# Kernel optimization log

Hardware: AMD Instinct MI355X
Metric: run time of the kernel (lower is better)

Reference implementation:

```python
import jax, jax.numpy as jnp
import numpy as np
import math

B, S, D, H, P = 4, 2048, 512, 8, 64
HD = D // H


def setup_inputs() -> dict:
    key = jax.random.key(0)
    ks = jax.random.split(key, 12)
    inp = {
        "query": jax.random.normal(ks[0], (B, S, D), jnp.float32),
        "key": jax.random.normal(ks[1], (B, S, D), jnp.float32),
        "value": jax.random.normal(ks[2], (B, S, D), jnp.float32),
        "query_pos_em": jax.random.normal(ks[3], (B, S, P), jnp.float32),
        "key_pos_em": jax.random.normal(ks[4], (B, S, P), jnp.float32),
        "mask": jax.random.randint(ks[5], (B, S), 0, 2, jnp.int32),
        # learned params (bias=False linears, LayerNorm affine)
        "Wq": jax.random.normal(ks[6], (D, D), jnp.float32) / math.sqrt(D),
        "Wk": jax.random.normal(ks[7], (D, D), jnp.float32) / math.sqrt(D),
        "Wv": jax.random.normal(ks[8], (D, D), jnp.float32) / math.sqrt(D),
        "Wo": jax.random.normal(ks[9], (D, D), jnp.float32) / math.sqrt(D),
        "ln_gamma": jnp.ones((D,), jnp.float32),
        "ln_beta": jnp.zeros((D,), jnp.float32),
    }
    return inp


def _split_heads(x):
    # (B,S,D) -> (B,H,S,HD)
    return x.reshape(B, S, H, HD).transpose(0, 2, 1, 3)


def reference(query, key, value, query_pos_em, key_pos_em, mask,
              Wq, Wk, Wv, Wo, ln_gamma, ln_beta):
    residual = query
    q = _split_heads(query @ Wq)
    k = _split_heads(key @ Wk)
    v = _split_heads(value @ Wv)

    # positional similarity: softmax over (B,S,S)
    simi = jax.nn.softmax(jnp.einsum('bqp,bkp->bqk', query_pos_em, key_pos_em), axis=-1)

    # scaled dot-product modulated elementwise by similarity (broadcast over heads)
    prod = jnp.einsum('bhqd,bhkd->bhqk', q, k) / math.sqrt(HD)
    prod = prod * simi[:, None, :, :]

    # additive mask: (mask-1)*1e8, broadcast [:, None, None, :]
    m = (mask.astype(prod.dtype) - 1.0) * 1e8
    prod = prod + m[:, None, None, :]

    attn = jax.nn.softmax(prod, axis=-1)
    out = jnp.einsum('bhqk,bhkd->bhqd', attn, v)  # (B,H,S,HD)
    out = out.transpose(0, 2, 1, 3).reshape(B, S, D)
    out = out @ Wo  # dropout is identity in eval mode

    x = residual + out
    mu = jnp.mean(x, axis=-1, keepdims=True)
    var = jnp.var(x, axis=-1, keepdims=True)
    return (x - mu) / jnp.sqrt(var + 1e-5) * ln_gamma + ln_beta
```

## Files before the change

kernel.cpp:

```cpp
#include <hip/hip_runtime.h>
#include <hip/hip_bf16.h>

#define Bq 4
#define Sq 2048
#define Dq 512
#define Hq 8
#define HDq 64
#define Pq 64

typedef __attribute__((ext_vector_type(8))) short short8;
typedef __attribute__((ext_vector_type(4))) float f32x4;

__device__ inline unsigned short f2bf(float f) {
  unsigned int u = __float_as_uint(f);
  unsigned int r = u + 0x7FFFu + ((u >> 16) & 1u);
  return (unsigned short)(r >> 16);
}
__device__ inline float bf2f(unsigned short s) {
  return __uint_as_float(((unsigned int)s) << 16);
}
__device__ inline short8 ld8f(const float* __restrict__ p) {
  const float4 a = *(const float4*)p;
  const float4 b = *(const float4*)(p + 4);
  short8 r;
  r[0] = (short)f2bf(a.x); r[1] = (short)f2bf(a.y); r[2] = (short)f2bf(a.z); r[3] = (short)f2bf(a.w);
  r[4] = (short)f2bf(b.x); r[5] = (short)f2bf(b.y); r[6] = (short)f2bf(b.z); r[7] = (short)f2bf(b.w);
  return r;
}

__global__ __launch_bounds__(256) void prep_conv(const float* __restrict__ qpe,
                                                 const float* __restrict__ kpe,
                                                 const int* __restrict__ mask,
                                                 const float* __restrict__ Wq,
                                                 const float* __restrict__ Wk,
                                                 const float* __restrict__ Wv,
                                                 const float* __restrict__ Wo,
                                                 unsigned short* __restrict__ qpeb,
                                                 unsigned short* __restrict__ kpeb,
                                                 float* __restrict__ mb,
                                                 unsigned short* __restrict__ Wqt,
                                                 unsigned short* __restrict__ Wkt,
                                                 unsigned short* __restrict__ Wvt,
                                                 unsigned short* __restrict__ Wot) {
  __shared__ float tile[32][33];
  const int bid = blockIdx.x;
  if (bid < 256) {
    int i = bid * 256 + threadIdx.x;
    *(short8*)&qpeb[(size_t)i * 8] = ld8f(qpe + (size_t)i * 8);
  } else if (bid < 512) {
    int i = (bid - 256) * 256 + threadIdx.x;
    *(short8*)&kpeb[(size_t)i * 8] = ld8f(kpe + (size_t)i * 8);
  } else if (bid < 544) {
    int i = (bid - 512) * 256 + threadIdx.x;
    mb[i] = ((float)mask[i] - 1.0f) * 1.442695041e8f;
  } else {
    const int cid = bid - 544;
    const int x = cid & 15, y = (cid >> 4) & 15, z = cid >> 8;
    const float* W = z == 0 ? Wq : z == 1 ? Wk : z == 2 ? Wv : Wo;
    unsigned short* Wt = z == 0 ? Wqt : z == 1 ? Wkt : z == 2 ? Wvt : Wot;
    const float scale = (z == 0) ? 0.125f : 1.0f;
    const int tx = threadIdx.x & 31, ty = threadIdx.x >> 5;
    const int n0 = x * 32, k0 = y * 32;
    for (int j = 0; j < 4; ++j)
      tile[ty + j * 8][tx] = W[(size_t)(k0 + ty + j * 8) * Dq + n0 + tx];
    __syncthreads();
    for (int j = 0; j < 4; ++j)
      Wt[(size_t)(n0 + ty + j * 8) * Dq + k0 + tx] = f2bf(tile[tx][ty + j * 8] * scale);
  }
}

__global__ __launch_bounds__(256) void gemm_qkv(const float* __restrict__ Aq,
                                                const float* __restrict__ Ak,
                                                const float* __restrict__ Av,
                                                const unsigned short* __restrict__ Wqt,
                                                const unsigned short* __restrict__ Wkt,
                                                const unsigned short* __restrict__ Wvt,
                                                unsigned short* __restrict__ Qb,
                                                unsigned short* __restrict__ Kb,
                                                unsigned short* __restrict__ VbT) {
  __shared__ unsigned short Alds[128][72];
  __shared__ unsigned short Blds[128][72];
  const int z = blockIdx.z;
  const float* Ap = z == 0 ? Aq : z == 1 ? Ak : Av;
  const unsigned short* Wt = z == 0 ? Wqt : z == 1 ? Wkt : Wvt;
  unsigned short* Cb = z == 0 ? Qb : z == 1 ? Kb : VbT;
  const bool wt = (z == 2);
  const int tid = threadIdx.x;
  const int lane = tid & 63, wv = tid >> 6;
  const int wr = wv >> 1, wc = wv & 1;
  const int l15 = lane & 15, lg = lane >> 4;
  const int row0 = blockIdx.x * 128, col0 = blockIdx.y * 128;
  f32x4 acc[4][4] = {};
  for (int k0 = 0; k0 < Dq; k0 += 64) {
    __syncthreads();
#pragma unroll
    for (int j = 0; j < 4; ++j) {
      int s = tid + j * 256;
      int r = s >> 3, c8 = (s & 7) * 8;
      const float* ap = Ap + (size_t)(row0 + r) * Dq + k0 + c8;
      float4 f0 = *(const float4*)ap;
      float4 f1 = *(const float4*)(ap + 4);
      short8 u;
      u[0] = (short)f2bf(f0.x); u[1] = (short)f2bf(f0.y);
      u[2] = (short)f2bf(f0.z); u[3] = (short)f2bf(f0.w);
      u[4] = (short)f2bf(f1.x); u[5] = (short)f2bf(f1.y);
      u[6] = (short)f2bf(f1.z); u[7] = (short)f2bf(f1.w);
      *(short8*)&Alds[r][c8] = u;
      *(uint4*)&Blds[r][c8] = *(const uint4*)&Wt[(size_t)(col0 + r) * Dq + k0 + c8];
    }
    __syncthreads();
#pragma unroll
    for (int kc = 0; kc < 2; ++kc) {
      short8 a[4], b[4];
#pragma unroll
      for (int mi = 0; mi < 4; ++mi)
        a[mi] = *(const short8*)&Alds[wr * 64 + mi * 16 + l15][kc * 32 + lg * 8];
#pragma unroll
      for (int ni = 0; ni < 4; ++ni)
        b[ni] = *(const short8*)&Blds[wc * 64 + ni * 16 + l15][kc * 32 + lg * 8];
#pragma unroll
      for (int mi = 0; mi < 4; ++mi)
#pragma unroll
        for (int ni = 0; ni < 4; ++ni)
          acc[mi][ni] = __builtin_amdgcn_mfma_f32_16x16x32_bf16(a[mi], b[ni], acc[mi][ni], 0, 0, 0);
    }
  }
  const int orow = row0 + wr * 64 + lg * 4;
  const int ocol = col0 + wc * 64 + l15;
  if (wt) {
    const int bidx = orow >> 11;
#pragma unroll
    for (int mi = 0; mi < 4; ++mi)
#pragma unroll
      for (int ni = 0; ni < 4; ++ni) {
        int gc = ocol + ni * 16;
        int s = (orow + mi * 16) & (Sq - 1);
        ushort4 w = {f2bf(acc[mi][ni][0]), f2bf(acc[mi][ni][1]),
                     f2bf(acc[mi][ni][2]), f2bf(acc[mi][ni][3])};
        *(ushort4*)&Cb[((size_t)(bidx * Dq + gc)) * Sq + s] = w;
      }
  } else {
#pragma unroll
    for (int mi = 0; mi < 4; ++mi)
#pragma unroll
      for (int ni = 0; ni < 4; ++ni)
#pragma unroll
        for (int rr = 0; rr < 4; ++rr) {
          int gr = orow + mi * 16 + rr, gc = ocol + ni * 16;
          Cb[(size_t)gr * Dq + gc] = f2bf(acc[mi][ni][rr]);
        }
  }
}

__global__ __launch_bounds__(256) void gemm_wo(const unsigned short* __restrict__ Ab,
                                               const unsigned short* __restrict__ Wt,
                                               const float* __restrict__ res,
                                               float* __restrict__ Cf) {
  __shared__ unsigned short Alds[128][72];
  __shared__ unsigned short Blds[128][72];
  const int tid = threadIdx.x;
  const int lane = tid & 63, wv = tid >> 6;
  const int wr = wv >> 1, wc = wv & 1;
  const int l15 = lane & 15, lg = lane >> 4;
  const int row0 = blockIdx.x * 128, col0 = blockIdx.y * 128;
  f32x4 acc[4][4] = {};
  for (int k0 = 0; k0 < Dq; k0 += 64) {
    __syncthreads();
#pragma unroll
    for (int j = 0; j < 4; ++j) {
      int s = tid + j * 256;
      int r = s >> 3, c8 = (s & 7) * 8;
      *(uint4*)&Alds[r][c8] = *(const uint4*)&Ab[(size_t)(row0 + r) * Dq + k0 + c8];
      *(uint4*)&Blds[r][c8] = *(const uint4*)&Wt[(size_t)(col0 + r) * Dq + k0 + c8];
    }
    __syncthreads();
#pragma unroll
    for (int kc = 0; kc < 2; ++kc) {
      short8 a[4], b[4];
#pragma unroll
      for (int mi = 0; mi < 4; ++mi)
        a[mi] = *(const short8*)&Alds[wr * 64 + mi * 16 + l15][kc * 32 + lg * 8];
#pragma unroll
      for (int ni = 0; ni < 4; ++ni)
        b[ni] = *(const short8*)&Blds[wc * 64 + ni * 16 + l15][kc * 32 + lg * 8];
#pragma unroll
      for (int mi = 0; mi < 4; ++mi)
#pragma unroll
        for (int ni = 0; ni < 4; ++ni)
          acc[mi][ni] = __builtin_amdgcn_mfma_f32_16x16x32_bf16(a[mi], b[ni], acc[mi][ni], 0, 0, 0);
    }
  }
  const int orow = row0 + wr * 64 + lg * 4;
  const int ocol = col0 + wc * 64 + l15;
#pragma unroll
  for (int mi = 0; mi < 4; ++mi)
#pragma unroll
    for (int ni = 0; ni < 4; ++ni)
#pragma unroll
      for (int rr = 0; rr < 4; ++rr) {
        int gr = orow + mi * 16 + rr, gc = ocol + ni * 16;
        Cf[(size_t)gr * Dq + gc] = acc[mi][ni][rr] + res[(size_t)gr * Dq + gc];
      }
}

__global__ __launch_bounds__(256) void possim(const unsigned short* __restrict__ qpe,
                                              const unsigned short* __restrict__ kpe,
                                              unsigned short* __restrict__ simiB,
                                              float* __restrict__ invsum) {
  __shared__ float wsum[4][16];
  const int tid = threadIdx.x, lane = tid & 63, wv = tid >> 6;
  const int l15 = lane & 15, lg = lane >> 4;
  const int b = blockIdx.y, q0 = blockIdx.x * 16;
  const unsigned short* qrow = qpe + ((size_t)(b * Sq + q0 + l15)) * Pq + lg * 8;
  short8 aq0 = *(const short8*)qrow;
  short8 aq1 = *(const short8*)(qrow + 32);
  unsigned short* sB = simiB + ((size_t)(b * (Sq / 16) + blockIdx.x)) * Sq * 16;
  float lsum[4] = {0.f, 0.f, 0.f, 0.f};
  for (int t = wv; t < Sq / 64; t += 4) {
    int k0 = t * 64;
    f32x4 sc[4] = {};
#pragma unroll
    for (int ng = 0; ng < 4; ++ng) {
      const unsigned short* krow = kpe + ((size_t)(b * Sq + k0 + ng * 16 + l15)) * Pq + lg * 8;
      short8 bk0 = *(const short8*)krow;
      short8 bk1 = *(const short8*)(krow + 32);
      sc[ng] = __builtin_amdgcn_mfma_f32_16x16x32_bf16(aq0, bk0, sc[ng], 0, 0, 0);
      sc[ng] = __builtin_amdgcn_mfma_f32_16x16x32_bf16(aq1, bk1, sc[ng], 0, 0, 0);
    }
#pragma unroll
    for (int ng = 0; ng < 4; ++ng) {
      float e0 = __expf(sc[ng][0]);
      float e1 = __expf(sc[ng][1]);
      float e2 = __expf(sc[ng][2]);
      float e3 = __expf(sc[ng][3]);
      lsum[0] += e0; lsum[1] += e1; lsum[2] += e2; lsum[3] += e3;
      ushort4 st = {f2bf(e0), f2bf(e1), f2bf(e2), f2bf(e3)};
      *(ushort4*)&sB[(size_t)(k0 + ng * 16 + l15) * 16 + lg * 4] = st;
    }
  }
  for (int rr = 0; rr < 4; ++rr)
    for (int m = 1; m < 16; m <<= 1) lsum[rr] += __shfl_xor(lsum[rr], m, 64);
  if (l15 == 0)
    for (int rr = 0; rr < 4; ++rr) wsum[wv][lg * 4 + rr] = lsum[rr];
  __syncthreads();
  if (tid < 16) {
    float tot = wsum[0][tid] + wsum[1][tid] + wsum[2][tid] + wsum[3][tid];
    invsum[b * Sq + q0 + tid] = 1.0f / tot;
  }
}

__global__ __launch_bounds__(512) void attn(const unsigned short* __restrict__ Qb,
                                            const unsigned short* __restrict__ Kb,
                                            const unsigned short* __restrict__ VbT,
                                            const unsigned short* __restrict__ simiB,
                                            const float* __restrict__ invsum,
                                            const float* __restrict__ mbias,
                                            unsigned short* __restrict__ O) {
  __shared__ unsigned short Klds[2][64][72];
  __shared__ unsigned short Vlds[2][64][72];
  __shared__ unsigned short Plds[8][16][72];
  const int tid = threadIdx.x, lane = tid & 63, wv = tid >> 6;
  const int l15 = lane & 15, lg = lane >> 4;
  const int q0 = blockIdx.x * 128, h = blockIdx.y, b = blockIdx.z;
  const int qw = q0 + wv * 16;
  const int sr = tid >> 3, sc8 = (tid & 7) * 8;
  const unsigned short* Kg = Kb + ((size_t)(b * Sq + sr)) * Dq + h * HDq + sc8;
  const unsigned short* Vg = VbT + ((size_t)(b * Dq + h * HDq + sr)) * Sq + sc8;

  const unsigned short* qp = Qb + ((size_t)(b * Sq + qw + l15)) * Dq + h * HDq + lg * 8;
  short8 aq0 = *(const short8*)qp;
  short8 aq1 = *(const short8*)(qp + 32);
  float inv2[4];
#pragma unroll
  for (int rr = 0; rr < 4; ++rr)
    inv2[rr] = invsum[b * Sq + qw + lg * 4 + rr] * 1.442695041f;
  const unsigned short* sB =
      simiB + ((size_t)(b * (Sq / 16) + blockIdx.x * 8 + wv)) * Sq * 16 + lg * 4;
  const float* Mb = mbias + b * Sq;

  ushort4 sv4[4];
  float mbf[4];
#pragma unroll
  for (int ng = 0; ng < 4; ++ng) {
    int kk = ng * 16 + l15;
    sv4[ng] = *(const ushort4*)&sB[(size_t)kk * 16];
    mbf[ng] = Mb[kk];
  }
  {
    *(uint4*)&Klds[0][sr][sc8] = *(const uint4*)Kg;
    *(uint4*)&Vlds[0][sr][sc8] = *(const uint4*)Vg;
  }
  f32x4 oacc[4] = {};
  float lsum[4] = {0.f, 0.f, 0.f, 0.f};
  int cur = 0;
  for (int t = 0; t < Sq / 64; ++t) {
    const int k0 = t * 64;
    __syncthreads();
    uint4 nk0, nv0;
    ushort4 nsv[4];
    float nmb[4];
    const bool more = (t < Sq / 64 - 1);
    if (more) {
      nk0 = *(const uint4*)(Kg + (size_t)(k0 + 64) * Dq);
      nv0 = *(const uint4*)(Vg + (k0 + 64));
#pragma unroll
      for (int ng = 0; ng < 4; ++ng) {
        int kk = k0 + 64 + ng * 16 + l15;
        nsv[ng] = *(const ushort4*)&sB[(size_t)kk * 16];
        nmb[ng] = Mb[kk];
      }
    }
    f32x4 sc[4] = {};
    __builtin_amdgcn_s_setprio(1);
#pragma unroll
    for (int ng = 0; ng < 4; ++ng) {
      short8 bk0 = *(const short8*)&Klds[cur][ng * 16 + l15][lg * 8];
      short8 bk1 = *(const short8*)&Klds[cur][ng * 16 + l15][32 + lg * 8];
      sc[ng] = __builtin_amdgcn_mfma_f32_16x16x32_bf16(aq0, bk0, sc[ng], 0, 0, 0);
      sc[ng] = __builtin_amdgcn_mfma_f32_16x16x32_bf16(aq1, bk1, sc[ng], 0, 0, 0);
    }
    __builtin_amdgcn_s_setprio(0);
#pragma unroll
    for (int ng = 0; ng < 4; ++ng) {
#pragma unroll
      for (int rr = 0; rr < 4; ++rr) {
        float sv = bf2f(rr == 0 ? sv4[ng].x : rr == 1 ? sv4[ng].y : rr == 2 ? sv4[ng].z
                                                                            : sv4[ng].w);
        float p = __builtin_amdgcn_exp2f(fmaf(sc[ng][rr] * sv, inv2[rr], mbf[ng]));
        lsum[rr] += p;
        Plds[wv][lg * 4 + rr][ng * 16 + l15] = f2bf(p);
      }
    }
    short8 pa0 = *(const short8*)&Plds[wv][l15][lg * 8];
    short8 pa1 = *(const short8*)&Plds[wv][l15][32 + lg * 8];
    __builtin_amdgcn_s_setprio(1);
#pragma unroll
    for (int dg = 0; dg < 4; ++dg) {
      short8 bv0 = *(const short8*)&Vlds[cur][dg * 16 + l15][lg * 8];
      short8 bv1 = *(const short8*)&Vlds[cur][dg * 16 + l15][32 + lg * 8];
      oacc[dg] = __builtin_amdgcn_mfma_f32_16x16x32_bf16(pa0, bv0, oacc[dg], 0, 0, 0);
      oacc[dg] = __builtin_amdgcn_mfma_f32_16x16x32_bf16(pa1, bv1, oacc[dg], 0, 0, 0);
    }
    __builtin_amdgcn_s_setprio(0);
    if (more) {
      *(uint4*)&Klds[cur ^ 1][sr][sc8] = nk0;
      *(uint4*)&Vlds[cur ^ 1][sr][sc8] = nv0;
#pragma unroll
      for (int ng = 0; ng < 4; ++ng) {
        sv4[ng] = nsv[ng];
        mbf[ng] = nmb[ng];
      }
      cur ^= 1;
    }
  }
#pragma unroll
  for (int rr = 0; rr < 4; ++rr)
    for (int m = 1; m < 16; m <<= 1) lsum[rr] += __shfl_xor(lsum[rr], m, 64);
#pragma unroll
  for (int dg = 0; dg < 4; ++dg)
    for (int rr = 0; rr < 4; ++rr) {
      int qg = qw + lg * 4 + rr;
      O[((size_t)(b * Sq + qg)) * Dq + h * HDq + dg * 16 + l15] = f2bf(oacc[dg][rr] / lsum[rr]);
    }
}

__global__ __launch_bounds__(256) void lnorm(float* __restrict__ X,
                                             const float* __restrict__ gamma,
                                             const float* __restrict__ beta) {
  const int tid = threadIdx.x, lane = tid & 63, wv = tid >> 6;
  const int row = blockIdx.x * 4 + wv;
  float* xr = X + (size_t)row * Dq + lane * 8;
  float4 x0 = *(float4*)xr;
  float4 x1 = *(float4*)(xr + 4);
  float s = x0.x + x0.y + x0.z + x0.w + x1.x + x1.y + x1.z + x1.w;
  float s2 = x0.x * x0.x + x0.y * x0.y + x0.z * x0.z + x0.w * x0.w +
             x1.x * x1.x + x1.y * x1.y + x1.z * x1.z + x1.w * x1.w;
  for (int m = 1; m < 64; m <<= 1) {
    s += __shfl_xor(s, m, 64);
    s2 += __shfl_xor(s2, m, 64);
  }
  float mu = s * (1.0f / 512.0f);
  float var = s2 * (1.0f / 512.0f) - mu * mu;
  float rstd = rsqrtf(var + 1e-5f);
  const float* g = gamma + lane * 8;
  const float* be = beta + lane * 8;
  float4 y0, y1;
  y0.x = (x0.x - mu) * rstd * g[0] + be[0];
  y0.y = (x0.y - mu) * rstd * g[1] + be[1];
  y0.z = (x0.z - mu) * rstd * g[2] + be[2];
  y0.w = (x0.w - mu) * rstd * g[3] + be[3];
  y1.x = (x1.x - mu) * rstd * g[4] + be[4];
  y1.y = (x1.y - mu) * rstd * g[5] + be[5];
  y1.z = (x1.z - mu) * rstd * g[6] + be[6];
  y1.w = (x1.w - mu) * rstd * g[7] + be[7];
  *(float4*)xr = y0;
  *(float4*)(xr + 4) = y1;
}

extern "C" void kernel_launch(void* const* d_in, const int* in_sizes, int n_in,
                              void* d_out, int out_size, void* d_ws, size_t ws_size,
                              hipStream_t stream) {
  const float* query = (const float*)d_in[0];
  const float* key = (const float*)d_in[1];
  const float* value = (const float*)d_in[2];
  const float* qpe = (const float*)d_in[3];
  const float* kpe = (const float*)d_in[4];
  const int* mask = (const int*)d_in[5];
  const float* Wq = (const float*)d_in[6];
  const float* Wk = (const float*)d_in[7];
  const float* Wv = (const float*)d_in[8];
  const float* Wo = (const float*)d_in[9];
  const float* gamma = (const float*)d_in[10];
  const float* beta = (const float*)d_in[11];
  float* out = (float*)d_out;

  char* ws = (char*)d_ws;
  size_t off = 0;
  unsigned short* Qb = (unsigned short*)(ws + off); off += (size_t)Bq * Sq * Dq * 2;
  unsigned short* Kb = (unsigned short*)(ws + off); off += (size_t)Bq * Sq * Dq * 2;
  unsigned short* VbT = (unsigned short*)(ws + off); off += (size_t)Bq * Sq * Dq * 2;
  unsigned short* Wqt = (unsigned short*)(ws + off); off += (size_t)Dq * Dq * 2;
  unsigned short* Wkt = (unsigned short*)(ws + off); off += (size_t)Dq * Dq * 2;
  unsigned short* Wvt = (unsigned short*)(ws + off); off += (size_t)Dq * Dq * 2;
  unsigned short* Wot = (unsigned short*)(ws + off); off += (size_t)Dq * Dq * 2;
  unsigned short* simiB = (unsigned short*)(ws + off); off += (size_t)Bq * Sq * Sq * 2;
  float* invsum = (float*)(ws + off); off += (size_t)Bq * Sq * 4;
  float* mbias = (float*)(ws + off); off += (size_t)Bq * Sq * 4;
  unsigned short* Ob = (unsigned short*)(ws + off); off += (size_t)Bq * Sq * Dq * 2;
  unsigned short* qpeb = (unsigned short*)(ws + off); off += (size_t)Bq * Sq * Pq * 2;
  unsigned short* kpeb = (unsigned short*)(ws + off); off += (size_t)Bq * Sq * Pq * 2;

  dim3 blk(256);
  prep_conv<<<dim3(544 + 1024), blk, 0, stream>>>(qpe, kpe, mask, Wq, Wk, Wv, Wo, qpeb, kpeb,
                                                  mbias, Wqt, Wkt, Wvt, Wot);
  possim<<<dim3(Sq / 16, Bq), blk, 0, stream>>>(qpeb, kpeb, simiB, invsum);
  gemm_qkv<<<dim3(64, 4, 3), blk, 0, stream>>>(query, key, value, Wqt, Wkt, Wvt, Qb, Kb, VbT);
  attn<<<dim3(Sq / 128, Hq, Bq), dim3(512), 0, stream>>>(Qb, Kb, VbT, simiB, invsum, mbias, Ob);
  gemm_wo<<<dim3(64, 4), blk, 0, stream>>>(Ob, Wot, query, out);
  lnorm<<<dim3(Bq * Sq / 4), blk, 0, stream>>>(out, gamma, beta);
}
```

Measured before the change: 148.6 us.

## Single-buffer K/V LDS tiles and load simi/mask per tile instead of prefetching

Replaces the double-buffered K/V shared-memory tiles with single buffers and adds a second barrier before overwriting them. The simi and mask values are now loaded at the start of each tile rather than prefetched one iteration ahead. This reduces LDS footprint and register pressure, presumably to raise occupancy. The cost is an extra __syncthreads per iteration and exposed global-load latency for the simi and mask values.

```diff
diff --git a/kernel.cpp b/kernel.cpp
--- a/kernel.cpp
+++ b/kernel.cpp
@@ -256,8 +256,8 @@
                                             const float* __restrict__ invsum,
                                             const float* __restrict__ mbias,
                                             unsigned short* __restrict__ O) {
-  __shared__ unsigned short Klds[2][64][72];
-  __shared__ unsigned short Vlds[2][64][72];
+  __shared__ unsigned short Klds[64][72];
+  __shared__ unsigned short Vlds[64][72];
   __shared__ unsigned short Plds[8][16][72];
   const int tid = threadIdx.x, lane = tid & 63, wv = tid >> 6;
   const int l15 = lane & 15, lg = lane >> 4;
@@ -278,44 +278,35 @@
       simiB + ((size_t)(b * (Sq / 16) + blockIdx.x * 8 + wv)) * Sq * 16 + lg * 4;
   const float* Mb = mbias + b * Sq;
 
-  ushort4 sv4[4];
-  float mbf[4];
-#pragma unroll
-  for (int ng = 0; ng < 4; ++ng) {
-    int kk = ng * 16 + l15;
-    sv4[ng] = *(const ushort4*)&sB[(size_t)kk * 16];
-    mbf[ng] = Mb[kk];
-  }
   {
-    *(uint4*)&Klds[0][sr][sc8] = *(const uint4*)Kg;
-    *(uint4*)&Vlds[0][sr][sc8] = *(const uint4*)Vg;
+    *(uint4*)&Klds[sr][sc8] = *(const uint4*)Kg;
+    *(uint4*)&Vlds[sr][sc8] = *(const uint4*)Vg;
   }
   f32x4 oacc[4] = {};
   float lsum[4] = {0.f, 0.f, 0.f, 0.f};
-  int cur = 0;
   for (int t = 0; t < Sq / 64; ++t) {
     const int k0 = t * 64;
     __syncthreads();
     uint4 nk0, nv0;
-    ushort4 nsv[4];
-    float nmb[4];
     const bool more = (t < Sq / 64 - 1);
     if (more) {
       nk0 = *(const uint4*)(Kg + (size_t)(k0 + 64) * Dq);
       nv0 = *(const uint4*)(Vg + (k0 + 64));
-#pragma unroll
-      for (int ng = 0; ng < 4; ++ng) {
-        int kk = k0 + 64 + ng * 16 + l15;
-        nsv[ng] = *(const ushort4*)&sB[(size_t)kk * 16];
-        nmb[ng] = Mb[kk];
-      }
+    }
+    ushort4 sv4[4];
+    float mbf[4];
+#pragma unroll
+    for (int ng = 0; ng < 4; ++ng) {
+      int kk = k0 + ng * 16 + l15;
+      sv4[ng] = *(const ushort4*)&sB[(size_t)kk * 16];
+      mbf[ng] = Mb[kk];
     }
     f32x4 sc[4] = {};
     __builtin_amdgcn_s_setprio(1);
 #pragma unroll
     for (int ng = 0; ng < 4; ++ng) {
-      short8 bk0 = *(const short8*)&Klds[cur][ng * 16 + l15][lg * 8];
-      short8 bk1 = *(const short8*)&Klds[cur][ng * 16 + l15][32 + lg * 8];
+      short8 bk0 = *(const short8*)&Klds[ng * 16 + l15][lg * 8];
+      short8 bk1 = *(const short8*)&Klds[ng * 16 + l15][32 + lg * 8];
       sc[ng] = __builtin_amdgcn_mfma_f32_16x16x32_bf16(aq0, bk0, sc[ng], 0, 0, 0);
       sc[ng] = __builtin_amdgcn_mfma_f32_16x16x32_bf16(aq1, bk1, sc[ng], 0, 0, 0);
     }
@@ -336,21 +327,16 @@
     __builtin_amdgcn_s_setprio(1);
 #pragma unroll
     for (int dg = 0; dg < 4; ++dg) {
-      short8 bv0 = *(const short8*)&Vlds[cur][dg * 16 + l15][lg * 8];
-      short8 bv1 = *(const short8*)&Vlds[cur][dg * 16 + l15][32 + lg * 8];
+      short8 bv0 = *(const short8*)&Vlds[dg * 16 + l15][lg * 8];
+      short8 bv1 = *(const short8*)&Vlds[dg * 16 + l15][32 + lg * 8];
       oacc[dg] = __builtin_amdgcn_mfma_f32_16x16x32_bf16(pa0, bv0, oacc[dg], 0, 0, 0);
       oacc[dg] = __builtin_amdgcn_mfma_f32_16x16x32_bf16(pa1, bv1, oacc[dg], 0, 0, 0);
     }
     __builtin_amdgcn_s_setprio(0);
+    __syncthreads();
     if (more) {
-      *(uint4*)&Klds[cur ^ 1][sr][sc8] = nk0;
-      *(uint4*)&Vlds[cur ^ 1][sr][sc8] = nv0;
-#pragma unroll
-      for (int ng = 0; ng < 4; ++ng) {
-        sv4[ng] = nsv[ng];
-        mbf[ng] = nmb[ng];
-      }
-      cur ^= 1;
+      *(uint4*)&Klds[sr][sc8] = nk0;
+      *(uint4*)&Vlds[sr][sc8] = nv0;
     }
   }
 #pragma unroll
```

Result: no change. 147.7 us (-0.6%).
